# Kernel tuning notes

Hardware: AMD Instinct MI355X
Metric: run time of the kernel (lower is better)

## Reference

```python
import jax, jax.numpy as jnp
import numpy as np

EPS = 1e-6

def _layernorm(x, g, b):
    m = jnp.mean(x, axis=-1, keepdims=True)
    v = jnp.var(x, axis=-1, keepdims=True)
    return (x - m) / jnp.sqrt(v + EPS) * g + b

def setup_inputs() -> dict:
    key = jax.random.key(0)
    ks = jax.random.split(key, 12)
    B, L, D, H = 2, 1024, 1024, 16
    s = 0.02  # weight init scale
    return {
        "query": jax.random.normal(ks[0], (B, L, D), jnp.float32),
        "pos_bias": jax.random.normal(ks[1], (H, L, L), jnp.float32) * 0.1,
        "postag_bias": jax.random.normal(ks[2], (B, H, L, L), jnp.float32) * 0.1,
        "lex_mask": jax.random.normal(ks[3], (B, L), jnp.float32) * 0.1,
        "mask": jax.random.randint(ks[4], (B, L), 0, 2).astype(jnp.int32),
        "Wq": jax.random.normal(ks[5], (D, D), jnp.float32) * s,
        "bq": jnp.zeros((D,), jnp.float32),
        "Wk": jax.random.normal(ks[6], (D, D), jnp.float32) * s,
        "bk": jnp.zeros((D,), jnp.float32),
        "Wv": jax.random.normal(ks[7], (D, D), jnp.float32) * s,
        "bv": jnp.zeros((D,), jnp.float32),
        "Wo": jax.random.normal(ks[8], (D, D), jnp.float32) * s,
        "bo": jnp.zeros((D,), jnp.float32),
        "gamma": jnp.ones((D,), jnp.float32),
        "beta": jnp.zeros((D,), jnp.float32),
    }

def reference(query, pos_bias, postag_bias, lex_mask, mask,
              Wq, bq, Wk, bk, Wv, bv, Wo, bo, gamma, beta):
    B, L, D = query.shape
    H = pos_bias.shape[0]
    dk = D // H
    scale = jnp.asarray(dk ** 0.5, query.dtype)

    residual = query
    context = query              # context=None path: set BEFORE pre-LN norm
    qn = _layernorm(query, gamma, beta)  # pre_ln=True applies only to query

    Q = (qn @ Wq.T + bq).reshape(B, L, H, dk)       # bqhd
    K = (context @ Wk.T + bk).reshape(B, L, H, dk)  # bkhd
    V = (context @ Wv.T + bv).reshape(B, L, H, dk)

    # (B,H,L,S) logits with all additive bias terms
    logits = jnp.einsum('bqhd,bkhd->bhqk', Q, K) / scale
    logits = logits + pos_bias[None]               # rel-pos bias (H,L,S)
    logits = logits + postag_bias                  # POS-tag bias (B,H,L,S)
    logits = logits + lex_mask[:, None, None, :]   # additive lexical mask
    logits = jnp.where(mask[:, None, None, :] == 0, -jnp.inf, logits)

    attn = jax.nn.softmax(logits, axis=-1)         # dropout inactive (eval)
    out = jnp.einsum('bhqk,bkhd->bqhd', attn, V).reshape(B, L, D)
    out = out @ Wo.T + bo
    out = out + residual
    return out, attn
```

## Files before the change

### kernel.cpp

```cpp
#include <hip/hip_runtime.h>
#include <hip/hip_bf16.h>
#include <math.h>

constexpr int B = 2, L = 1024, D = 1024, H = 16, DK = 64;
constexpr int M = B * L;
constexpr int DD = D * D;

typedef __attribute__((ext_vector_type(8))) short bf16x8;
typedef __attribute__((ext_vector_type(4))) float f32x4;

__device__ inline unsigned short f2bf(float f) {
    __hip_bfloat16 h = __float2bfloat16(f);
    return __builtin_bit_cast(unsigned short, h);
}

__device__ inline void glds16(const void* g, void* l) {
    __builtin_amdgcn_global_load_lds((const __attribute__((address_space(1))) void*)g,
                                     (__attribute__((address_space(3))) void*)l,
                                     16, 0, 0);
}

__global__ __launch_bounds__(256) void ln2_kernel(const float* __restrict__ x,
                                                  const float* __restrict__ gamma,
                                                  const float* __restrict__ beta,
                                                  unsigned short* __restrict__ qn16,
                                                  unsigned short* __restrict__ q16) {
    int row = blockIdx.x;
    int t = threadIdx.x;
    const float4 v = ((const float4*)(x + (size_t)row * D))[t];
    float s  = v.x + v.y + v.z + v.w;
    float sq = v.x*v.x + v.y*v.y + v.z*v.z + v.w*v.w;
    #pragma unroll
    for (int m = 32; m >= 1; m >>= 1) {
        s  += __shfl_xor(s, m, 64);
        sq += __shfl_xor(sq, m, 64);
    }
    __shared__ float rs[4], rq[4];
    int wid = t >> 6;
    if ((t & 63) == 0) { rs[wid] = s; rq[wid] = sq; }
    __syncthreads();
    s  = rs[0] + rs[1] + rs[2] + rs[3];
    sq = rq[0] + rq[1] + rq[2] + rq[3];
    float mean = s * (1.0f / D);
    float var  = sq * (1.0f / D) - mean * mean;
    float rstd = rsqrtf(var + 1e-6f);
    float4 g  = ((const float4*)gamma)[t];
    float4 bb = ((const float4*)beta)[t];
    ushort4 on, oq;
    on.x = f2bf((v.x - mean) * rstd * g.x + bb.x);
    on.y = f2bf((v.y - mean) * rstd * g.y + bb.y);
    on.z = f2bf((v.z - mean) * rstd * g.z + bb.z);
    on.w = f2bf((v.w - mean) * rstd * g.w + bb.w);
    oq.x = f2bf(v.x); oq.y = f2bf(v.y); oq.z = f2bf(v.z); oq.w = f2bf(v.w);
    ((ushort4*)(qn16 + (size_t)row * D))[t] = on;
    ((ushort4*)(q16  + (size_t)row * D))[t] = oq;
}

__global__ __launch_bounds__(256) void wconv_kernel(const float* __restrict__ Wq,
                                                    const float* __restrict__ Wk,
                                                    const float* __restrict__ Wv,
                                                    const float* __restrict__ Wo,
                                                    unsigned short* __restrict__ out) {
    const float* src = (blockIdx.y == 0) ? Wq : (blockIdx.y == 1) ? Wk
                       : (blockIdx.y == 2) ? Wv : Wo;
    size_t i = (size_t)blockIdx.x * 256 + threadIdx.x;
    float4 v = ((const float4*)src)[i];
    ushort4 o;
    o.x = f2bf(v.x); o.y = f2bf(v.y); o.z = f2bf(v.z); o.w = f2bf(v.w);
    ((ushort4*)(out + (size_t)blockIdx.y * DD))[i] = o;
}

__global__ __launch_bounds__(256) void gemm_qkv(
        const unsigned short* __restrict__ qn16, const unsigned short* __restrict__ q16,
        const unsigned short* __restrict__ W,
        const float* __restrict__ bq, const float* __restrict__ bk,
        const float* __restrict__ bv,
        unsigned short* __restrict__ Qm, unsigned short* __restrict__ Km,
        unsigned short* __restrict__ Vm) {
    __shared__ __align__(16) unsigned short As[128 * 64];
    __shared__ __align__(16) unsigned short Ws[128 * 64];
    int t = threadIdx.x, lane = t & 63, w = t >> 6;
    int quad = lane >> 4, l15 = lane & 15;
    int nt = blockIdx.x;
    int bm = blockIdx.y * 128;
    const unsigned short* A = (nt < 8) ? qn16 : q16;
    const float* bias = (nt < 8) ? bq : ((nt < 16) ? bk : bv);
    unsigned short* Cout = (nt < 8) ? Qm : ((nt < 16) ? Km : Vm);
    int bn_local = (nt & 7) * 128;
    int wm = (w >> 1) * 64, wn = (w & 1) * 64;
    f32x4 acc[4][4] = {};
    for (int k0 = 0; k0 < D; k0 += 64) {
        __syncthreads();
        const unsigned short* ap = A + (size_t)(bm + w * 32) * D + k0;
        const unsigned short* wp = W + (size_t)(nt * 128 + w * 32) * D + k0;
        #pragma unroll
        for (int i = 0; i < 4; i++) {
            int c = i * 64 + lane;
            int r = c >> 3, g = (c & 7) ^ (r & 7);
            glds16(ap + (size_t)r * D + g * 8, &As[w * 2048 + i * 512]);
            glds16(wp + (size_t)r * D + g * 8, &Ws[w * 2048 + i * 512]);
        }
        __syncthreads();
        #pragma unroll
        for (int k2 = 0; k2 < 2; k2++) {
            bf16x8 av[4], bw[4];
            #pragma unroll
            for (int i = 0; i < 4; i++) {
                int r = wm + i * 16 + l15;
                av[i] = *(const bf16x8*)&As[r * 64 + (((quad + 4 * k2) ^ (r & 7)) * 8)];
            }
            #pragma unroll
            for (int j = 0; j < 4; j++) {
                int r = wn + j * 16 + l15;
                bw[j] = *(const bf16x8*)&Ws[r * 64 + (((quad + 4 * k2) ^ (r & 7)) * 8)];
            }
            #pragma unroll
            for (int i = 0; i < 4; i++)
                #pragma unroll
                for (int j = 0; j < 4; j++)
                    acc[i][j] = __builtin_amdgcn_mfma_f32_16x16x32_bf16(av[i], bw[j], acc[i][j], 0, 0, 0);
        }
    }
    #pragma unroll
    for (int j = 0; j < 4; j++) {
        int col = bn_local + wn + j * 16 + l15;
        float bcol = bias[col];
        #pragma unroll
        for (int i = 0; i < 4; i++)
            #pragma unroll
            for (int rg = 0; rg < 4; rg++) {
                int row = bm + wm + i * 16 + quad * 4 + rg;
                Cout[(size_t)row * D + col] = f2bf(acc[i][j][rg] + bcol);
            }
    }
}

__global__ __launch_bounds__(256) void vtrans_kernel(const unsigned short* __restrict__ Vm,
                                                     unsigned short* __restrict__ Vt) {
    __shared__ unsigned short sb[128 * 66];
    int t = threadIdx.x;
    int z = blockIdx.y;
    int b = z >> 4, h = z & 15;
    int s0 = blockIdx.x * 128;
    size_t base = (size_t)b * L * D + (size_t)h * 64;
    #pragma unroll
    for (int i = 0; i < 4; i++) {
        int idx = t + 256 * i;
        int r = idx >> 3, c8 = idx & 7;
        uint4 vv = *(const uint4*)&Vm[base + (size_t)(s0 + r) * D + c8 * 8];
        unsigned int* sp = (unsigned int*)&sb[r * 66 + c8 * 8];
        sp[0] = vv.x; sp[1] = vv.y; sp[2] = vv.z; sp[3] = vv.w;
    }
    __syncthreads();
    #pragma unroll
    for (int i = 0; i < 4; i++) {
        int idx = t + 256 * i;
        int d = idx >> 4, sc = idx & 15;
        unsigned short tmp[8];
        #pragma unroll
        for (int j = 0; j < 8; j++) tmp[j] = sb[(sc * 8 + j) * 66 + d];
        *(uint4*)&Vt[((size_t)z * 64 + d) * L + s0 + sc * 8] = *(uint4*)tmp;
    }
}

__global__ __launch_bounds__(256) void attn4_kernel(
        const unsigned short* __restrict__ Qm, const unsigned short* __restrict__ Km,
        const float* __restrict__ pos_bias, const float* __restrict__ postag,
        const float* __restrict__ lex, const int* __restrict__ mask,
        float* __restrict__ attn_out) {
    __shared__ __align__(16) unsigned short q_sh[16][72];
    __shared__ __align__(16) unsigned short kv_sh[128 * 64];
    __shared__ float redA[16][4], redB[16][4];

    int t = threadIdx.x, lane = t & 63, w = t >> 6;
    int quad = lane >> 4, l15 = lane & 15;
    int qt = blockIdx.x & 63;
    int bh = blockIdx.x >> 6;
    int b = bh >> 4, h = bh & 15;
    int q0 = qt * 16;
    int q = q0 + l15;
    size_t base = (size_t)b * L * D + (size_t)h * DK;

    if (t < 128) {
        int r = t >> 3, c8 = t & 7;
        *(uint4*)&q_sh[r][c8 * 8] = *(const uint4*)&Qm[base + (size_t)(q0 + r) * D + c8 * 8];
    }
    __syncthreads();
    bf16x8 qb0 = *(const bf16x8*)&q_sh[l15][quad * 8];
    bf16x8 qb1 = *(const bf16x8*)&q_sh[l15][32 + quad * 8];

    f32x4 acc[16] = {};
    for (int st = 0; st < 8; st++) {
        __syncthreads();
        const unsigned short* kp = Km + base + (size_t)(st * 128 + w * 32) * D;
        #pragma unroll
        for (int i = 0; i < 4; i++) {
            int c = i * 64 + lane;
            int r = c >> 3, g = (c & 7) ^ (r & 7);
            glds16(kp + (size_t)r * D + g * 8, &kv_sh[w * 2048 + i * 512]);
        }
        __syncthreads();
        #pragma unroll
        for (int u = 0; u < 2; u++) {
            int r = (u * 4 + w) * 16 + l15;
            bf16x8 ka0 = *(const bf16x8*)&kv_sh[r * 64 + ((quad ^ (r & 7)) * 8)];
            bf16x8 ka1 = *(const bf16x8*)&kv_sh[r * 64 + (((quad + 4) ^ (r & 7)) * 8)];
            int ti = 2 * st + u;
            acc[ti] = __builtin_amdgcn_mfma_f32_16x16x32_bf16(ka0, qb0, acc[ti], 0, 0, 0);
            acc[ti] = __builtin_amdgcn_mfma_f32_16x16x32_bf16(ka1, qb1, acc[ti], 0, 0, 0);
        }
    }
    #pragma unroll
    for (int ti = 0; ti < 16; ti++) {
        int nt = (ti >> 1) * 8 + (ti & 1) * 4 + w;
        int s0 = nt * 16 + quad * 4;
        float4 pb = *(const float4*)&pos_bias[((size_t)h * L + q) * L + s0];
        float4 pt = *(const float4*)&postag[((size_t)bh * L + q) * L + s0];
        float4 lx = *(const float4*)&lex[b * L + s0];
        int4   mk = *(const int4*)&mask[b * L + s0];
        acc[ti][0] = mk.x ? acc[ti][0] * 0.125f + pb.x + pt.x + lx.x : -1e30f;
        acc[ti][1] = mk.y ? acc[ti][1] * 0.125f + pb.y + pt.y + lx.y : -1e30f;
        acc[ti][2] = mk.z ? acc[ti][2] * 0.125f + pb.z + pt.z + lx.z : -1e30f;
        acc[ti][3] = mk.w ? acc[ti][3] * 0.125f + pb.w + pt.w + lx.w : -1e30f;
    }
    float mx = -1e30f;
    #pragma unroll
    for (int ti = 0; ti < 16; ti++)
        #pragma unroll
        for (int rg = 0; rg < 4; rg++) mx = fmaxf(mx, acc[ti][rg]);
    mx = fmaxf(mx, __shfl_xor(mx, 16, 64));
    mx = fmaxf(mx, __shfl_xor(mx, 32, 64));
    if (quad == 0) redA[l15][w] = mx;
    __syncthreads();
    mx = fmaxf(fmaxf(redA[l15][0], redA[l15][1]), fmaxf(redA[l15][2], redA[l15][3]));
    float sum = 0.f;
    #pragma unroll
    for (int ti = 0; ti < 16; ti++)
        #pragma unroll
        for (int rg = 0; rg < 4; rg++) {
            float e = __expf(acc[ti][rg] - mx);
            acc[ti][rg] = e;
            sum += e;
        }
    sum += __shfl_xor(sum, 16, 64);
    sum += __shfl_xor(sum, 32, 64);
    if (quad == 0) redB[l15][w] = sum;
    __syncthreads();
    float inv = 1.0f / (redB[l15][0] + redB[l15][1] + redB[l15][2] + redB[l15][3]);
    #pragma unroll
    for (int ti = 0; ti < 16; ti++) {
        int nt = (ti >> 1) * 8 + (ti & 1) * 4 + w;
        int s0 = nt * 16 + quad * 4;
        float4 o;
        o.x = acc[ti][0] * inv; o.y = acc[ti][1] * inv;
        o.z = acc[ti][2] * inv; o.w = acc[ti][3] * inv;
        *(float4*)&attn_out[((size_t)bh * L + q) * L + s0] = o;
    }
}

__global__ __launch_bounds__(256) void gemm_pv(
        const float* __restrict__ attnP, const unsigned short* __restrict__ Vt,
        unsigned short* __restrict__ ctx16) {
    __shared__ __align__(16) unsigned short As[64][72];
    __shared__ __align__(16) unsigned short Ws[64 * 64];
    int t = threadIdx.x, lane = t & 63, w = t >> 6;
    int quad = lane >> 4, l15 = lane & 15;
    int bm = blockIdx.x * 64, z = blockIdx.z;
    int wm = (w >> 1) * 32, wn = (w & 1) * 32;
    int ar = t >> 2, ac = (t & 3) * 16;
    f32x4 acc[2][2] = {};
    for (int k0 = 0; k0 < L; k0 += 64) {
        __syncthreads();
        const unsigned short* wp = Vt + ((size_t)z * 64 + w * 16) * L + k0;
        #pragma unroll
        for (int i = 0; i < 2; i++) {
            int c = i * 64 + lane;
            int r = c >> 3, g = (c & 7) ^ (r & 7);
            glds16(wp + (size_t)r * L + g * 8, &Ws[w * 1024 + i * 512]);
        }
        {
            const float* ap = &attnP[((size_t)z * L + bm + ar) * L + k0 + ac];
            float4 f0 = *(const float4*)ap;
            float4 f1 = *(const float4*)(ap + 4);
            float4 f2 = *(const float4*)(ap + 8);
            float4 f3 = *(const float4*)(ap + 12);
            ushort4 u0, u1, u2, u3;
            u0.x = f2bf(f0.x); u0.y = f2bf(f0.y); u0.z = f2bf(f0.z); u0.w = f2bf(f0.w);
            u1.x = f2bf(f1.x); u1.y = f2bf(f1.y); u1.z = f2bf(f1.z); u1.w = f2bf(f1.w);
            u2.x = f2bf(f2.x); u2.y = f2bf(f2.y); u2.z = f2bf(f2.z); u2.w = f2bf(f2.w);
            u3.x = f2bf(f3.x); u3.y = f2bf(f3.y); u3.z = f2bf(f3.z); u3.w = f2bf(f3.w);
            *(ushort4*)&As[ar][ac]      = u0;
            *(ushort4*)&As[ar][ac + 4]  = u1;
            *(ushort4*)&As[ar][ac + 8]  = u2;
            *(ushort4*)&As[ar][ac + 12] = u3;
        }
        __syncthreads();
        #pragma unroll
        for (int k2 = 0; k2 < 2; k2++) {
            bf16x8 av[2], bw[2];
            #pragma unroll
            for (int i = 0; i < 2; i++)
                av[i] = *(const bf16x8*)&As[wm + i * 16 + l15][k2 * 32 + quad * 8];
            #pragma unroll
            for (int j = 0; j < 2; j++) {
                int r = wn + j * 16 + l15;
                bw[j] = *(const bf16x8*)&Ws[r * 64 + (((quad + 4 * k2) ^ (r & 7)) * 8)];
            }
            #pragma unroll
            for (int i = 0; i < 2; i++)
                #pragma unroll
                for (int j = 0; j < 2; j++)
                    acc[i][j] = __builtin_amdgcn_mfma_f32_16x16x32_bf16(av[i], bw[j], acc[i][j], 0, 0, 0);
        }
    }
    size_t coff = (size_t)(z >> 4) * L * D + (size_t)(z & 15) * 64;
    #pragma unroll
    for (int i = 0; i < 2; i++)
        #pragma unroll
        for (int j = 0; j < 2; j++)
            #pragma unroll
            for (int rg = 0; rg < 4; rg++) {
                int row = bm + wm + i * 16 + quad * 4 + rg;
                int col = wn + j * 16 + l15;
                ctx16[coff + (size_t)row * D + col] = f2bf(acc[i][j][rg]);
            }
}

__global__ __launch_bounds__(256) void gemm_out(
        const unsigned short* __restrict__ A, const unsigned short* __restrict__ W,
        const float* __restrict__ bias, const float* __restrict__ res,
        float* __restrict__ C) {
    __shared__ __align__(16) unsigned short As[64 * 64];
    __shared__ __align__(16) unsigned short Ws[64 * 64];
    int t = threadIdx.x, lane = t & 63, w = t >> 6;
    int quad = lane >> 4, l15 = lane & 15;
    int bm = blockIdx.x * 64, bn = blockIdx.y * 64;
    int wm = (w >> 1) * 32, wn = (w & 1) * 32;
    f32x4 acc[2][2] = {};
    for (int k0 = 0; k0 < D; k0 += 64) {
        __syncthreads();
        const unsigned short* ap = A + (size_t)(bm + w * 16) * D + k0;
        const unsigned short* wp = W + (size_t)(bn + w * 16) * D + k0;
        #pragma unroll
        for (int i = 0; i < 2; i++) {
            int c = i * 64 + lane;
            int r = c >> 3, g = (c & 7) ^ (r & 7);
            glds16(ap + (size_t)r * D + g * 8, &As[w * 1024 + i * 512]);
            glds16(wp + (size_t)r * D + g * 8, &Ws[w * 1024 + i * 512]);
        }
        __syncthreads();
        #pragma unroll
        for (int k2 = 0; k2 < 2; k2++) {
            bf16x8 av[2], bw[2];
            #pragma unroll
            for (int i = 0; i < 2; i++) {
                int r = wm + i * 16 + l15;
                av[i] = *(const bf16x8*)&As[r * 64 + (((quad + 4 * k2) ^ (r & 7)) * 8)];
            }
            #pragma unroll
            for (int j = 0; j < 2; j++) {
                int r = wn + j * 16 + l15;
                bw[j] = *(const bf16x8*)&Ws[r * 64 + (((quad + 4 * k2) ^ (r & 7)) * 8)];
            }
            #pragma unroll
            for (int i = 0; i < 2; i++)
                #pragma unroll
                for (int j = 0; j < 2; j++)
                    acc[i][j] = __builtin_amdgcn_mfma_f32_16x16x32_bf16(av[i], bw[j], acc[i][j], 0, 0, 0);
        }
    }
    #pragma unroll
    for (int j = 0; j < 2; j++) {
        int col = bn + wn + j * 16 + l15;
        float bcol = bias[col];
        #pragma unroll
        for (int i = 0; i < 2; i++)
            #pragma unroll
            for (int rg = 0; rg < 4; rg++) {
                int row = bm + wm + i * 16 + quad * 4 + rg;
                C[(size_t)row * D + col] = acc[i][j][rg] + bcol + res[(size_t)row * D + col];
            }
    }
}

extern "C" void kernel_launch(void* const* d_in, const int* in_sizes, int n_in,
                              void* d_out, int out_size, void* d_ws, size_t ws_size,
                              hipStream_t stream) {
    (void)in_sizes; (void)n_in; (void)out_size; (void)ws_size;
    const float* query  = (const float*)d_in[0];
    const float* pos_b  = (const float*)d_in[1];
    const float* postag = (const float*)d_in[2];
    const float* lex    = (const float*)d_in[3];
    const int*   mask   = (const int*)d_in[4];
    const float* Wq = (const float*)d_in[5];
    const float* bq = (const float*)d_in[6];
    const float* Wk = (const float*)d_in[7];
    const float* bk = (const float*)d_in[8];
    const float* Wv = (const float*)d_in[9];
    const float* bv = (const float*)d_in[10];
    const float* Wo = (const float*)d_in[11];
    const float* bo = (const float*)d_in[12];
    const float* gamma = (const float*)d_in[13];
    const float* beta  = (const float*)d_in[14];

    float* out  = (float*)d_out;
    float* attn = out + (size_t)B * L * D;

    unsigned short* ws16 = (unsigned short*)d_ws;
    const size_t NE = (size_t)M * D;
    unsigned short* qn16  = ws16;
    unsigned short* q16   = ws16 + NE;
    unsigned short* W16   = ws16 + 2 * NE;
    unsigned short* Qm16  = W16 + 4 * (size_t)DD;
    unsigned short* Km16  = Qm16 + NE;
    unsigned short* Vm16  = Km16 + NE;
    unsigned short* Vt16  = Vm16 + NE;
    unsigned short* ctx16 = Vt16 + NE;

    ln2_kernel<<<M, 256, 0, stream>>>(query, gamma, beta, qn16, q16);
    wconv_kernel<<<dim3(DD / 1024, 4), 256, 0, stream>>>(Wq, Wk, Wv, Wo, W16);
    gemm_qkv<<<dim3(24, 16), 256, 0, stream>>>(qn16, q16, W16, bq, bk, bv,
                                               Qm16, Km16, Vm16);
    vtrans_kernel<<<dim3(8, 32), 256, 0, stream>>>(Vm16, Vt16);
    attn4_kernel<<<B * H * (L / 16), 256, 0, stream>>>(Qm16, Km16, pos_b, postag,
                                                       lex, mask, attn);
    gemm_pv<<<dim3(16, 1, 32), 256, 0, stream>>>(attn, Vt16, ctx16);
    gemm_out<<<dim3(32, 16), 256, 0, stream>>>(ctx16, W16 + 3 * (size_t)DD, bo, query, out);
}
```

Baseline: 499.5 us.

## Interleave bias loads with QK tile loop and premerge lex/mask into LDS

Moves the pos_bias and postag bias loads into the K-tile loop so they are issued alongside the K async copies and applied right after each tile's MFMAs, overlapping global latency with compute. A new small kernel folds the lexical mask and padding mask into a single additive array, which the attention kernel stages in shared memory. It also adds an occupancy hint in launch bounds. The masked value becomes -1e30 plus the bias terms rather than exactly -1e30, and the extra kernel launch adds overhead.

```diff
diff --git a/kernel.cpp b/kernel.cpp
--- a/kernel.cpp
+++ b/kernel.cpp
@@ -68,6 +68,13 @@
     ushort4 o;
     o.x = f2bf(v.x); o.y = f2bf(v.y); o.z = f2bf(v.z); o.w = f2bf(v.w);
     ((ushort4*)(out + (size_t)blockIdx.y * DD))[i] = o;
+}
+
+__global__ __launch_bounds__(256) void lsm_kernel(const float* __restrict__ lex,
+                                                  const int* __restrict__ mask,
+                                                  float* __restrict__ lsm) {
+    int i = blockIdx.x * 256 + threadIdx.x;
+    lsm[i] = mask[i] ? lex[i] : -1e30f;
 }
 
 __global__ __launch_bounds__(256) void gemm_qkv(
@@ -163,13 +170,13 @@
     }
 }
 
-__global__ __launch_bounds__(256) void attn4_kernel(
+__global__ __launch_bounds__(256, 4) void attn4_kernel(
         const unsigned short* __restrict__ Qm, const unsigned short* __restrict__ Km,
         const float* __restrict__ pos_bias, const float* __restrict__ postag,
-        const float* __restrict__ lex, const int* __restrict__ mask,
-        float* __restrict__ attn_out) {
+        const float* __restrict__ lsm, float* __restrict__ attn_out) {
     __shared__ __align__(16) unsigned short q_sh[16][72];
     __shared__ __align__(16) unsigned short kv_sh[128 * 64];
+    __shared__ float lsm_sh[1024];
     __shared__ float redA[16][4], redB[16][4];
 
     int t = threadIdx.x, lane = t & 63, w = t >> 6;
@@ -185,9 +192,13 @@
         int r = t >> 3, c8 = t & 7;
         *(uint4*)&q_sh[r][c8 * 8] = *(const uint4*)&Qm[base + (size_t)(q0 + r) * D + c8 * 8];
     }
+    ((float4*)lsm_sh)[t] = ((const float4*)(lsm + b * L))[t];
     __syncthreads();
     bf16x8 qb0 = *(const bf16x8*)&q_sh[l15][quad * 8];
     bf16x8 qb1 = *(const bf16x8*)&q_sh[l15][32 + quad * 8];
+
+    const float* pbp = pos_bias + ((size_t)h * L + q) * L;
+    const float* ptp = postag + ((size_t)bh * L + q) * L;
 
     f32x4 acc[16] = {};
     for (int st = 0; st < 8; st++) {
@@ -199,6 +210,12 @@
             int r = c >> 3, g = (c & 7) ^ (r & 7);
             glds16(kp + (size_t)r * D + g * 8, &kv_sh[w * 2048 + i * 512]);
         }
+        int s_u0 = st * 128 + w * 16 + quad * 4;
+        int s_u1 = s_u0 + 64;
+        float4 pb0 = *(const float4*)(pbp + s_u0);
+        float4 pt0 = *(const float4*)(ptp + s_u0);
+        float4 pb1 = *(const float4*)(pbp + s_u1);
+        float4 pt1 = *(const float4*)(ptp + s_u1);
         __syncthreads();
         #pragma unroll
         for (int u = 0; u < 2; u++) {
@@ -209,19 +226,20 @@
             acc[ti] = __builtin_amdgcn_mfma_f32_16x16x32_bf16(ka0, qb0, acc[ti], 0, 0, 0);
             acc[ti] = __builtin_amdgcn_mfma_f32_16x16x32_bf16(ka1, qb1, acc[ti], 0, 0, 0);
         }
-    }
-    #pragma unroll
-    for (int ti = 0; ti < 16; ti++) {
-        int nt = (ti >> 1) * 8 + (ti & 1) * 4 + w;
-        int s0 = nt * 16 + quad * 4;
-        float4 pb = *(const float4*)&pos_bias[((size_t)h * L + q) * L + s0];
-        float4 pt = *(const float4*)&postag[((size_t)bh * L + q) * L + s0];
-        float4 lx = *(const float4*)&lex[b * L + s0];
-        int4   mk = *(const int4*)&mask[b * L + s0];
-        acc[ti][0] = mk.x ? acc[ti][0] * 0.125f + pb.x + pt.x + lx.x : -1e30f;
-        acc[ti][1] = mk.y ? acc[ti][1] * 0.125f + pb.y + pt.y + lx.y : -1e30f;
-        acc[ti][2] = mk.z ? acc[ti][2] * 0.125f + pb.z + pt.z + lx.z : -1e30f;
-        acc[ti][3] = mk.w ? acc[ti][3] * 0.125f + pb.w + pt.w + lx.w : -1e30f;
+        {
+            int ti = 2 * st;
+            float4 l0 = *(const float4*)&lsm_sh[s_u0];
+            acc[ti][0] = acc[ti][0] * 0.125f + (pb0.x + pt0.x + l0.x);
+            acc[ti][1] = acc[ti][1] * 0.125f + (pb0.y + pt0.y + l0.y);
+            acc[ti][2] = acc[ti][2] * 0.125f + (pb0.z + pt0.z + l0.z);
+            acc[ti][3] = acc[ti][3] * 0.125f + (pb0.w + pt0.w + l0.w);
+            ti = 2 * st + 1;
+            float4 l1 = *(const float4*)&lsm_sh[s_u1];
+            acc[ti][0] = acc[ti][0] * 0.125f + (pb1.x + pt1.x + l1.x);
+            acc[ti][1] = acc[ti][1] * 0.125f + (pb1.y + pt1.y + l1.y);
+            acc[ti][2] = acc[ti][2] * 0.125f + (pb1.z + pt1.z + l1.z);
+            acc[ti][3] = acc[ti][3] * 0.125f + (pb1.w + pt1.w + l1.w);
+        }
     }
     float mx = -1e30f;
     #pragma unroll
@@ -249,8 +267,7 @@
     float inv = 1.0f / (redB[l15][0] + redB[l15][1] + redB[l15][2] + redB[l15][3]);
     #pragma unroll
     for (int ti = 0; ti < 16; ti++) {
-        int nt = (ti >> 1) * 8 + (ti & 1) * 4 + w;
-        int s0 = nt * 16 + quad * 4;
+        int s0 = (ti >> 1) * 128 + (ti & 1) * 64 + w * 16 + quad * 4;
         float4 o;
         o.x = acc[ti][0] * inv; o.y = acc[ti][1] * inv;
         o.z = acc[ti][2] * inv; o.w = acc[ti][3] * inv;
@@ -416,14 +433,16 @@
     unsigned short* Vm16  = Km16 + NE;
     unsigned short* Vt16  = Vm16 + NE;
     unsigned short* ctx16 = Vt16 + NE;
+    float* lsm = (float*)(ctx16 + NE);
 
     ln2_kernel<<<M, 256, 0, stream>>>(query, gamma, beta, qn16, q16);
     wconv_kernel<<<dim3(DD / 1024, 4), 256, 0, stream>>>(Wq, Wk, Wv, Wo, W16);
+    lsm_kernel<<<M / 256, 256, 0, stream>>>(lex, mask, lsm);
     gemm_qkv<<<dim3(24, 16), 256, 0, stream>>>(qn16, q16, W16, bq, bk, bv,
                                                Qm16, Km16, Vm16);
     vtrans_kernel<<<dim3(8, 32), 256, 0, stream>>>(Vm16, Vt16);
     attn4_kernel<<<B * H * (L / 16), 256, 0, stream>>>(Qm16, Km16, pos_b, postag,
-                                                       lex, mask, attn);
+                                                       lsm, attn);
     gemm_pv<<<dim3(16, 1, 32), 256, 0, stream>>>(attn, Vt16, ctx16);
     gemm_out<<<dim3(32, 16), 256, 0, stream>>>(ctx16, W16 + 3 * (size_t)DD, bo, query, out);
 }
```

New measurement: 418.8 us. 16.2% less time.
